# Optimization experiments

Measured on AMD Instinct MI355X. Metric: run time of the kernel, lower is better.

The kernel has to match this reference:

```python
import jax, jax.numpy as jnp
import numpy as np

N_HEADS = 8
D_MODEL = 256
HEAD_DEPTH = D_MODEL // N_HEADS
B, S = 2, 4096


def setup_inputs() -> dict:
    key = jax.random.key(0)
    ks = jax.random.split(key, 8)
    scale = 1.0 / np.sqrt(D_MODEL)
    return {
        "q": jax.random.normal(ks[0], (B, S, D_MODEL), dtype=jnp.float32),
        "k": jax.random.normal(ks[1], (B, S, D_MODEL), dtype=jnp.float32),
        "v": jax.random.normal(ks[2], (B, S, D_MODEL), dtype=jnp.float32),
        "mask": jax.random.randint(ks[3], (B, S, S), 0, 2).astype(jnp.bool_),
        "wq": jax.random.normal(ks[4], (D_MODEL, D_MODEL), dtype=jnp.float32) * scale,
        "wk": jax.random.normal(ks[5], (D_MODEL, D_MODEL), dtype=jnp.float32) * scale,
        "wv": jax.random.normal(ks[6], (D_MODEL, D_MODEL), dtype=jnp.float32) * scale,
        "w_out": jax.random.normal(ks[7], (D_MODEL, D_MODEL), dtype=jnp.float32) * scale,
    }


def _split_heads(x):
    # [B, S, D] -> [B, H, S, Dh]
    b, s, _ = x.shape
    return x.reshape(b, s, N_HEADS, HEAD_DEPTH).transpose(0, 2, 1, 3)


def reference(q, k, v, mask, wq, wk, wv, w_out):
    Q = _split_heads(q @ wq)
    K = _split_heads(k @ wk)
    V = _split_heads(v @ wv)
    # [B, H, Sq, Sk]
    scores = jnp.einsum('bhqd,bhkd->bhqk', Q, K) / jnp.sqrt(
        jnp.asarray(HEAD_DEPTH, dtype=Q.dtype))
    # mask True -> -inf, broadcast over heads
    scores = jnp.where(mask[:, None, :, :], -jnp.inf, scores)
    probs = jax.nn.softmax(scores, axis=-1)
    attn = jnp.einsum('bhqk,bhkd->bhqd', probs, V)
    attn = attn.transpose(0, 2, 1, 3).reshape(q.shape[0], -1, D_MODEL)
    return attn @ w_out
```

## Files before the change

### kernel.cpp

```cpp
#include <hip/hip_runtime.h>
#include <stdint.h>

typedef __bf16 bf16;
typedef __bf16 bf16x8 __attribute__((ext_vector_type(8)));
typedef __bf16 bf16x4 __attribute__((ext_vector_type(4)));
typedef float  f32x4  __attribute__((ext_vector_type(4)));
typedef float  float4v __attribute__((ext_vector_type(4)));

#define B_  2
#define S_  4096
#define H_  8
#define DH_ 32
#define D_  256

#define QSCALE 0.25505003984214403f

__global__ __launch_bounds__(256) void transpose_w(
    const float* __restrict__ w0, const float* __restrict__ w1,
    const float* __restrict__ w2, const float* __restrict__ w3,
    bf16* __restrict__ WT) {
  const int wsel = blockIdx.z;
  const float* W = wsel == 0 ? w0 : wsel == 1 ? w1 : wsel == 2 ? w2 : w3;
  const int k0 = blockIdx.x * 64, n0 = blockIdx.y * 64;
  __shared__ __align__(16) bf16 t[64][72];
  const int tid = threadIdx.x;
  {
    const int kk = (tid >> 4) << 2;
    const int nn = (tid & 15) << 2;
#pragma unroll
    for (int r = 0; r < 4; ++r) {
      float4v a = *(const float4v*)(W + (size_t)(k0 + kk + r) * 256 + n0 + nn);
#pragma unroll
      for (int j = 0; j < 4; ++j) t[nn + j][kk + r] = (bf16)a[j];
    }
  }
  __syncthreads();
  {
    const int ni = tid >> 2;
    const int c  = (tid & 3) * 16;
    bf16x8 o0 = *(const bf16x8*)(&t[ni][c]);
    bf16x8 o1 = *(const bf16x8*)(&t[ni][c + 8]);
    bf16* dst = WT + (size_t)wsel * 65536 + (size_t)(n0 + ni) * 256 + k0 + c;
    *(bf16x8*)dst = o0;
    *(bf16x8*)(dst + 8) = o1;
  }
}

__global__ __launch_bounds__(256) void pack_mask(const int* __restrict__ mask,
                                                 unsigned long long* __restrict__ out) {
  const int gw = blockIdx.x * 4 + (threadIdx.x >> 6);
  const int lane = threadIdx.x & 63;
  const int m = mask[(size_t)gw * 64 + lane];
  const unsigned long long bits = __ballot(m != 0);
  if (lane == 0) out[gw] = bits;
}

__global__ __launch_bounds__(256) void proj_kernel(
    const float* __restrict__ xq, const float* __restrict__ xk, const float* __restrict__ xv,
    const bf16* __restrict__ WT,
    bf16* __restrict__ Qo, bf16* __restrict__ Ko, bf16* __restrict__ Vo) {
  const int z = blockIdx.z;
  const float* X = z == 0 ? xq : (z == 1 ? xk : xv);
  const bf16* wt = WT + (size_t)z * 65536;
  const int m0 = blockIdx.x * 64, n0 = blockIdx.y * 128;
  const int tid = threadIdx.x, wave = tid >> 6, lane = tid & 63;
  const int nl = lane & 15, quad = lane >> 4;
  const int arow = m0 + wave * 16 + nl;
  const float* xrow = X + (size_t)arow * 256;

  f32x4 zero4 = {0.f, 0.f, 0.f, 0.f};
  f32x4 acc[8];
#pragma unroll
  for (int i = 0; i < 8; ++i) acc[i] = zero4;

  for (int ks = 0; ks < 8; ++ks) {
    float4v a0 = *(const float4v*)(xrow + ks * 32 + quad * 8);
    float4v a1 = *(const float4v*)(xrow + ks * 32 + quad * 8 + 4);
    bf16x8 af;
#pragma unroll
    for (int i = 0; i < 4; ++i) { af[i] = (bf16)a0[i]; af[4 + i] = (bf16)a1[i]; }
#pragma unroll
    for (int nf = 0; nf < 8; ++nf) {
      bf16x8 bfr = *(const bf16x8*)(wt + (size_t)(n0 + nf * 16 + nl) * 256 + ks * 32 + quad * 8);
      acc[nf] = __builtin_amdgcn_mfma_f32_16x16x32_bf16(af, bfr, acc[nf], 0, 0, 0);
    }
  }

  const float scale = (z == 0) ? QSCALE : 1.0f;
  bf16* Out = z == 0 ? Qo : (z == 1 ? Ko : Vo);
  const int Rbase = m0 + wave * 16 + quad * 4;
#pragma unroll
  for (int nf = 0; nf < 8; ++nf) {
    const int col = n0 + nf * 16 + nl;
    const int h = col >> 5, d = col & 31;
#pragma unroll
    for (int r = 0; r < 4; ++r) {
      const int R = Rbase + r;
      const int b = R >> 12, s = R & 4095;
      Out[(((size_t)(b * 8 + h)) * 4096 + s) * 32 + d] = (bf16)(acc[nf][r] * scale);
    }
  }
}

__global__ __launch_bounds__(256) void transpose_v(const bf16* __restrict__ Vi,
                                                   bf16* __restrict__ Vt) {
  const int bh = blockIdx.y;
  const int s0 = blockIdx.x * 64;
  __shared__ __align__(16) bf16 t[32][72];
  const int tid = threadIdx.x;
  const int si = tid >> 2, dc = (tid & 3) * 8;
  bf16x8 v = *(const bf16x8*)(Vi + ((size_t)bh * 4096 + s0 + si) * 32 + dc);
#pragma unroll
  for (int j = 0; j < 8; ++j) t[dc + j][si] = v[j];
  __syncthreads();
  const int d = tid >> 3, c = (tid & 7) * 8;
  bf16x8 o = *(const bf16x8*)(&t[d][c]);
  *(bf16x8*)(Vt + ((size_t)bh * 32 + d) * 4096 + s0 + c) = o;
}

__global__ __launch_bounds__(256) void attn_kernel(
    const bf16* __restrict__ Qg, const bf16* __restrict__ Kg,
    const bf16* __restrict__ Vtg, const unsigned long long* __restrict__ Mg,
    bf16* __restrict__ Og) {
  const int bh = blockIdx.y, b = bh >> 3, h = bh & 7;
  const int q0 = blockIdx.x * 64;
  const int tid = threadIdx.x, wave = tid >> 6, lane = tid & 63;
  const int nl = lane & 15, quad = lane >> 4;

  __shared__ __align__(16) bf16 Klds[64 * 32];
  __shared__ __align__(16) bf16 Vlds[32 * 80];
  __shared__ __align__(16) bf16 Plds[4][16 * 72];

  const int qrow = q0 + wave * 16 + nl;
  const bf16x8 qf = *(const bf16x8*)(Qg + ((size_t)bh * 4096 + qrow) * 32 + quad * 8);
  const unsigned long long* mrow = Mg + ((size_t)b * 4096 + qrow) * 64;
  const bf16* Kbase = Kg + (size_t)bh * 4096 * 32;
  const bf16* Vbase = Vtg + (size_t)bh * 32 * 4096;
  const int sd = tid >> 3, scn = (tid & 7) * 8;

  f32x4 zero4 = {0.f, 0.f, 0.f, 0.f};
  f32x4 acc0 = zero4, acc1 = zero4;
  float lsum = 0.f;

  bf16* pw = &Plds[wave][nl * 72 + 4 * quad];
  const bf16* pr = &Plds[wave][nl * 72 + quad * 8];

  for (int kt = 0; kt < 64; ++kt) {
    *(bf16x8*)(Klds + tid * 8) = *(const bf16x8*)(Kbase + (size_t)kt * 2048 + tid * 8);
    *(bf16x8*)(Vlds + sd * 80 + scn) = *(const bf16x8*)(Vbase + (size_t)sd * 4096 + kt * 64 + scn);
    __syncthreads();

    const unsigned long long mw = mrow[kt];

    f32x4 st[4];
#pragma unroll
    for (int t = 0; t < 4; ++t) {
      bf16x8 a = *(const bf16x8*)(Klds + (t * 16 + nl) * 32 + quad * 8);
      st[t] = __builtin_amdgcn_mfma_f32_16x16x32_bf16(a, qf, zero4, 0, 0, 0);
    }

#pragma unroll
    for (int t = 0; t < 4; ++t) {
      bf16x4 p4;
#pragma unroll
      for (int r = 0; r < 4; ++r) {
        const int kl = t * 16 + quad * 4 + r;
        float e = __builtin_amdgcn_exp2f(st[t][r]);
        e = ((mw >> kl) & 1ull) ? 0.f : e;
        lsum += e;
        p4[r] = (bf16)e;
      }
      *(bf16x4*)(pw + 16 * t) = p4;
    }

#pragma unroll
    for (int c = 0; c < 2; ++c) {
      bf16x8 pb  = *(const bf16x8*)(pr + c * 32);
      bf16x8 va0 = *(const bf16x8*)(Vlds + nl * 80 + c * 32 + quad * 8);
      bf16x8 va1 = *(const bf16x8*)(Vlds + (nl + 16) * 80 + c * 32 + quad * 8);
      acc0 = __builtin_amdgcn_mfma_f32_16x16x32_bf16(va0, pb, acc0, 0, 0, 0);
      acc1 = __builtin_amdgcn_mfma_f32_16x16x32_bf16(va1, pb, acc1, 0, 0, 0);
    }
    __syncthreads();
  }

  lsum += __shfl_xor(lsum, 16, 64);
  lsum += __shfl_xor(lsum, 32, 64);
  const float rl = 1.f / lsum;

  bf16x4 o0, o1;
#pragma unroll
  for (int r = 0; r < 4; ++r) { o0[r] = (bf16)(acc0[r] * rl); o1[r] = (bf16)(acc1[r] * rl); }
  bf16* obase = Og + ((size_t)(b * 4096 + qrow)) * 256 + h * 32 + quad * 4;
  *(bf16x4*)obase = o0;
  *(bf16x4*)(obase + 16) = o1;
}

__global__ __launch_bounds__(256) void gemm_out(
    const bf16* __restrict__ A, const bf16* __restrict__ WTo, float* __restrict__ C) {
  const int m0 = blockIdx.x * 64, n0 = blockIdx.y * 128;
  const int tid = threadIdx.x, wave = tid >> 6, lane = tid & 63;
  const int nl = lane & 15, quad = lane >> 4;
  const int arow = m0 + wave * 16 + nl;

  f32x4 zero4 = {0.f, 0.f, 0.f, 0.f};
  f32x4 acc[8];
#pragma unroll
  for (int i = 0; i < 8; ++i) acc[i] = zero4;

  for (int ks = 0; ks < 8; ++ks) {
    bf16x8 af = *(const bf16x8*)(A + (size_t)arow * 256 + ks * 32 + quad * 8);
#pragma unroll
    for (int nf = 0; nf < 8; ++nf) {
      bf16x8 bfr = *(const bf16x8*)(WTo + (size_t)(n0 + nf * 16 + nl) * 256 + ks * 32 + quad * 8);
      acc[nf] = __builtin_amdgcn_mfma_f32_16x16x32_bf16(af, bfr, acc[nf], 0, 0, 0);
    }
  }
  const int Rbase = m0 + wave * 16 + quad * 4;
#pragma unroll
  for (int nf = 0; nf < 8; ++nf)
#pragma unroll
    for (int r = 0; r < 4; ++r)
      C[(size_t)(Rbase + r) * 256 + n0 + nf * 16 + nl] = acc[nf][r];
}

extern "C" void kernel_launch(void* const* d_in, const int* in_sizes, int n_in,
                              void* d_out, int out_size, void* d_ws, size_t ws_size,
                              hipStream_t stream) {
  const float* q  = (const float*)d_in[0];
  const float* k  = (const float*)d_in[1];
  const float* v  = (const float*)d_in[2];
  const int*  mask = (const int*)d_in[3];
  const float* wq = (const float*)d_in[4];
  const float* wk = (const float*)d_in[5];
  const float* wv = (const float*)d_in[6];
  const float* wo = (const float*)d_in[7];
  float* out = (float*)d_out;

  uint8_t* ws = (uint8_t*)d_ws;
  bf16* WT = (bf16*)ws;
  bf16* Qb = (bf16*)(ws + (512u << 10));
  bf16* Kb = Qb + 2097152;
  bf16* Vb = Kb + 2097152;
  bf16* Vt = Vb + 2097152;
  unsigned long long* Mb = (unsigned long long*)((uint8_t*)(Vt + 2097152));
  bf16* Ao = (bf16*)((uint8_t*)Mb + (4u << 20));

  transpose_w<<<dim3(4, 4, 4), 256, 0, stream>>>(wq, wk, wv, wo, WT);
  pack_mask<<<dim3(131072), 256, 0, stream>>>(mask, Mb);
  proj_kernel<<<dim3(128, 2, 3), 256, 0, stream>>>(q, k, v, WT, Qb, Kb, Vb);
  transpose_v<<<dim3(64, 16), 256, 0, stream>>>(Vb, Vt);
  attn_kernel<<<dim3(64, 16), 256, 0, stream>>>(Qb, Kb, Vt, Mb, Ao);
  gemm_out<<<dim3(128, 2), 256, 0, stream>>>(Ao, WT + 3 * 65536, out);
}
```

Measured before the change: 378.3 us.

## Fuse V transpose into projection, widen attention K tile, batch mask packing

The V projection now writes directly in transposed layout, so the separate transpose_v kernel and its buffer are gone. The attention kernel processes 128 keys per iteration, which halves the number of barriers. It masks with a bitfield AND instead of a select and computes the softmax denominator with an extra MFMA against a ones vector instead of a scalar sum and shuffles. pack_mask has each wave ballot 16 words and store them with wide writes, cutting the block count from 131072 to 8192. The changes add LDS use and an extra MFMA per chunk, and the row sum is now accumulated from bf16-rounded probabilities.

```diff
diff --git a/kernel.cpp b/kernel.cpp
--- a/kernel.cpp
+++ b/kernel.cpp
@@ -6,12 +6,8 @@
 typedef __bf16 bf16x4 __attribute__((ext_vector_type(4)));
 typedef float  f32x4  __attribute__((ext_vector_type(4)));
 typedef float  float4v __attribute__((ext_vector_type(4)));
-
-#define B_  2
-#define S_  4096
-#define H_  8
-#define DH_ 32
-#define D_  256
+typedef unsigned int uint;
+typedef unsigned long long ull;
 
 #define QSCALE 0.25505003984214403f
 
@@ -47,18 +43,24 @@
 }
 
 __global__ __launch_bounds__(256) void pack_mask(const int* __restrict__ mask,
-                                                 unsigned long long* __restrict__ out) {
-  const int gw = blockIdx.x * 4 + (threadIdx.x >> 6);
+                                                 ull* __restrict__ out) {
+  const int wid = blockIdx.x * 4 + (threadIdx.x >> 6);
   const int lane = threadIdx.x & 63;
-  const int m = mask[(size_t)gw * 64 + lane];
-  const unsigned long long bits = __ballot(m != 0);
-  if (lane == 0) out[gw] = bits;
+  const size_t base = (size_t)wid * 1024 + lane;
+  ull b[16];
+#pragma unroll
+  for (int j = 0; j < 16; ++j) b[j] = __ballot(mask[base + 64 * j] != 0);
+  if (lane == 0) {
+    ulonglong2* o = (ulonglong2*)(out + (size_t)wid * 16);
+#pragma unroll
+    for (int j = 0; j < 8; ++j) { ulonglong2 v; v.x = b[2 * j]; v.y = b[2 * j + 1]; o[j] = v; }
+  }
 }
 
 __global__ __launch_bounds__(256) void proj_kernel(
     const float* __restrict__ xq, const float* __restrict__ xk, const float* __restrict__ xv,
     const bf16* __restrict__ WT,
-    bf16* __restrict__ Qo, bf16* __restrict__ Ko, bf16* __restrict__ Vo) {
+    bf16* __restrict__ Qo, bf16* __restrict__ Ko, bf16* __restrict__ Vt) {
   const int z = blockIdx.z;
   const float* X = z == 0 ? xq : (z == 1 ? xk : xv);
   const bf16* wt = WT + (size_t)z * 65536;
@@ -86,112 +88,121 @@
     }
   }
 
-  const float scale = (z == 0) ? QSCALE : 1.0f;
-  bf16* Out = z == 0 ? Qo : (z == 1 ? Ko : Vo);
   const int Rbase = m0 + wave * 16 + quad * 4;
-#pragma unroll
-  for (int nf = 0; nf < 8; ++nf) {
-    const int col = n0 + nf * 16 + nl;
-    const int h = col >> 5, d = col & 31;
-#pragma unroll
-    for (int r = 0; r < 4; ++r) {
-      const int R = Rbase + r;
-      const int b = R >> 12, s = R & 4095;
-      Out[(((size_t)(b * 8 + h)) * 4096 + s) * 32 + d] = (bf16)(acc[nf][r] * scale);
-    }
-  }
-}
-
-__global__ __launch_bounds__(256) void transpose_v(const bf16* __restrict__ Vi,
-                                                   bf16* __restrict__ Vt) {
-  const int bh = blockIdx.y;
-  const int s0 = blockIdx.x * 64;
-  __shared__ __align__(16) bf16 t[32][72];
-  const int tid = threadIdx.x;
-  const int si = tid >> 2, dc = (tid & 3) * 8;
-  bf16x8 v = *(const bf16x8*)(Vi + ((size_t)bh * 4096 + s0 + si) * 32 + dc);
-#pragma unroll
-  for (int j = 0; j < 8; ++j) t[dc + j][si] = v[j];
-  __syncthreads();
-  const int d = tid >> 3, c = (tid & 7) * 8;
-  bf16x8 o = *(const bf16x8*)(&t[d][c]);
-  *(bf16x8*)(Vt + ((size_t)bh * 32 + d) * 4096 + s0 + c) = o;
-}
-
-__global__ __launch_bounds__(256) void attn_kernel(
+  if (z == 2) {
+    const int b = Rbase >> 12, s = Rbase & 4095;
+#pragma unroll
+    for (int nf = 0; nf < 8; ++nf) {
+      const int col = n0 + nf * 16 + nl;
+      const int h = col >> 5, d = col & 31;
+      bf16x4 o;
+#pragma unroll
+      for (int r = 0; r < 4; ++r) o[r] = (bf16)acc[nf][r];
+      *(bf16x4*)(Vt + (((size_t)(b * 8 + h)) * 32 + d) * 4096 + s) = o;
+    }
+  } else {
+    const float scale = (z == 0) ? QSCALE : 1.0f;
+    bf16* Out = z == 0 ? Qo : Ko;
+#pragma unroll
+    for (int nf = 0; nf < 8; ++nf) {
+      const int col = n0 + nf * 16 + nl;
+      const int h = col >> 5, d = col & 31;
+#pragma unroll
+      for (int r = 0; r < 4; ++r) {
+        const int R = Rbase + r;
+        const int b = R >> 12, s = R & 4095;
+        Out[(((size_t)(b * 8 + h)) * 4096 + s) * 32 + d] = (bf16)(acc[nf][r] * scale);
+      }
+    }
+  }
+}
+
+__global__ __launch_bounds__(256, 6) void attn_kernel(
     const bf16* __restrict__ Qg, const bf16* __restrict__ Kg,
-    const bf16* __restrict__ Vtg, const unsigned long long* __restrict__ Mg,
+    const bf16* __restrict__ Vtg, const uint* __restrict__ Mg,
     bf16* __restrict__ Og) {
   const int bh = blockIdx.y, b = bh >> 3, h = bh & 7;
   const int q0 = blockIdx.x * 64;
   const int tid = threadIdx.x, wave = tid >> 6, lane = tid & 63;
-  const int nl = lane & 15, quad = lane >> 4;
-
-  __shared__ __align__(16) bf16 Klds[64 * 32];
-  __shared__ __align__(16) bf16 Vlds[32 * 80];
+  const int nl = lane & 15, quad = lane >> 4, q4 = quad * 4;
+
+  __shared__ __align__(16) bf16 Klds[128 * 32];
+  __shared__ __align__(16) bf16 Vlds[32 * 136];
   __shared__ __align__(16) bf16 Plds[4][16 * 72];
 
   const int qrow = q0 + wave * 16 + nl;
   const bf16x8 qf = *(const bf16x8*)(Qg + ((size_t)bh * 4096 + qrow) * 32 + quad * 8);
-  const unsigned long long* mrow = Mg + ((size_t)b * 4096 + qrow) * 64;
+  const uint* mrow = Mg + ((size_t)b * 4096 + qrow) * 128;
   const bf16* Kbase = Kg + (size_t)bh * 4096 * 32;
   const bf16* Vbase = Vtg + (size_t)bh * 32 * 4096;
-  const int sd = tid >> 3, scn = (tid & 7) * 8;
 
   f32x4 zero4 = {0.f, 0.f, 0.f, 0.f};
-  f32x4 acc0 = zero4, acc1 = zero4;
-  float lsum = 0.f;
-
-  bf16* pw = &Plds[wave][nl * 72 + 4 * quad];
+  f32x4 acc0 = zero4, acc1 = zero4, accl = zero4;
+  bf16x8 ones;
+#pragma unroll
+  for (int i = 0; i < 8; ++i) ones[i] = (bf16)1.0f;
+
+  bf16* pw = &Plds[wave][nl * 72 + q4];
   const bf16* pr = &Plds[wave][nl * 72 + quad * 8];
-
-  for (int kt = 0; kt < 64; ++kt) {
-    *(bf16x8*)(Klds + tid * 8) = *(const bf16x8*)(Kbase + (size_t)kt * 2048 + tid * 8);
-    *(bf16x8*)(Vlds + sd * 80 + scn) = *(const bf16x8*)(Vbase + (size_t)sd * 4096 + kt * 64 + scn);
+  const int vd = tid >> 4, vk = (tid & 15) * 8;
+
+  for (int kt = 0; kt < 32; ++kt) {
+    const bf16* kc = Kbase + kt * 4096;
+    *(bf16x8*)(Klds + tid * 8)        = *(const bf16x8*)(kc + tid * 8);
+    *(bf16x8*)(Klds + 2048 + tid * 8) = *(const bf16x8*)(kc + 2048 + tid * 8);
+    const bf16* vc = Vbase + kt * 128 + vk;
+    *(bf16x8*)(Vlds + vd * 136 + vk)        = *(const bf16x8*)(vc + (size_t)vd * 4096);
+    *(bf16x8*)(Vlds + (vd + 16) * 136 + vk) = *(const bf16x8*)(vc + (size_t)(vd + 16) * 4096);
     __syncthreads();
 
-    const unsigned long long mw = mrow[kt];
-
-    f32x4 st[4];
-#pragma unroll
-    for (int t = 0; t < 4; ++t) {
-      bf16x8 a = *(const bf16x8*)(Klds + (t * 16 + nl) * 32 + quad * 8);
-      st[t] = __builtin_amdgcn_mfma_f32_16x16x32_bf16(a, qf, zero4, 0, 0, 0);
-    }
-
-#pragma unroll
-    for (int t = 0; t < 4; ++t) {
-      bf16x4 p4;
-#pragma unroll
-      for (int r = 0; r < 4; ++r) {
-        const int kl = t * 16 + quad * 4 + r;
-        float e = __builtin_amdgcn_exp2f(st[t][r]);
-        e = ((mw >> kl) & 1ull) ? 0.f : e;
-        lsum += e;
-        p4[r] = (bf16)e;
-      }
-      *(bf16x4*)(pw + 16 * t) = p4;
-    }
-
-#pragma unroll
-    for (int c = 0; c < 2; ++c) {
-      bf16x8 pb  = *(const bf16x8*)(pr + c * 32);
-      bf16x8 va0 = *(const bf16x8*)(Vlds + nl * 80 + c * 32 + quad * 8);
-      bf16x8 va1 = *(const bf16x8*)(Vlds + (nl + 16) * 80 + c * 32 + quad * 8);
-      acc0 = __builtin_amdgcn_mfma_f32_16x16x32_bf16(va0, pb, acc0, 0, 0, 0);
-      acc1 = __builtin_amdgcn_mfma_f32_16x16x32_bf16(va1, pb, acc1, 0, 0, 0);
+    const uint4 mq = *(const uint4*)(mrow + kt * 4);
+
+#pragma unroll
+    for (int h2 = 0; h2 < 2; ++h2) {
+      const uint ks0 = (~(h2 ? mq.z : mq.x)) >> q4;
+      const uint ks1 = (~(h2 ? mq.w : mq.y)) >> q4;
+
+      f32x4 st[4];
+#pragma unroll
+      for (int t = 0; t < 4; ++t) {
+        bf16x8 a = *(const bf16x8*)(Klds + ((h2 * 4 + t) * 16 + nl) * 32 + quad * 8);
+        st[t] = __builtin_amdgcn_mfma_f32_16x16x32_bf16(a, qf, zero4, 0, 0, 0);
+      }
+
+#pragma unroll
+      for (int t = 0; t < 4; ++t) {
+        const uint ks = (t < 2) ? ks0 : ks1;
+        const int off = (t & 1) * 16;
+        bf16x4 p4;
+#pragma unroll
+        for (int r = 0; r < 4; ++r) {
+          float e = __builtin_amdgcn_exp2f(st[t][r]);
+          uint keep = (uint)__builtin_amdgcn_sbfe((int)ks, off + r, 1);
+          e = __uint_as_float(__float_as_uint(e) & keep);
+          p4[r] = (bf16)e;
+        }
+        *(bf16x4*)(pw + 16 * t) = p4;
+      }
+
+#pragma unroll
+      for (int c = 0; c < 2; ++c) {
+        bf16x8 pb  = *(const bf16x8*)(pr + c * 32);
+        bf16x8 va0 = *(const bf16x8*)(Vlds + nl * 136 + h2 * 64 + c * 32 + quad * 8);
+        bf16x8 va1 = *(const bf16x8*)(Vlds + (nl + 16) * 136 + h2 * 64 + c * 32 + quad * 8);
+        acc0 = __builtin_amdgcn_mfma_f32_16x16x32_bf16(va0, pb, acc0, 0, 0, 0);
+        acc1 = __builtin_amdgcn_mfma_f32_16x16x32_bf16(va1, pb, acc1, 0, 0, 0);
+        accl = __builtin_amdgcn_mfma_f32_16x16x32_bf16(ones, pb, accl, 0, 0, 0);
+      }
     }
     __syncthreads();
   }
 
-  lsum += __shfl_xor(lsum, 16, 64);
-  lsum += __shfl_xor(lsum, 32, 64);
-  const float rl = 1.f / lsum;
+  const float rl = 1.0f / accl[0];
 
   bf16x4 o0, o1;
 #pragma unroll
   for (int r = 0; r < 4; ++r) { o0[r] = (bf16)(acc0[r] * rl); o1[r] = (bf16)(acc1[r] * rl); }
-  bf16* obase = Og + ((size_t)(b * 4096 + qrow)) * 256 + h * 32 + quad * 4;
+  bf16* obase = Og + ((size_t)(b * 4096 + qrow)) * 256 + h * 32 + q4;
   *(bf16x4*)obase = o0;
   *(bf16x4*)(obase + 16) = o1;
 }
@@ -241,15 +252,13 @@
   bf16* WT = (bf16*)ws;
   bf16* Qb = (bf16*)(ws + (512u << 10));
   bf16* Kb = Qb + 2097152;
-  bf16* Vb = Kb + 2097152;
-  bf16* Vt = Vb + 2097152;
-  unsigned long long* Mb = (unsigned long long*)((uint8_t*)(Vt + 2097152));
+  bf16* Vt = Kb + 2097152;
+  ull*  Mb = (ull*)((uint8_t*)(Vt + 2097152));
   bf16* Ao = (bf16*)((uint8_t*)Mb + (4u << 20));
 
   transpose_w<<<dim3(4, 4, 4), 256, 0, stream>>>(wq, wk, wv, wo, WT);
-  pack_mask<<<dim3(131072), 256, 0, stream>>>(mask, Mb);
-  proj_kernel<<<dim3(128, 2, 3), 256, 0, stream>>>(q, k, v, WT, Qb, Kb, Vb);
-  transpose_v<<<dim3(64, 16), 256, 0, stream>>>(Vb, Vt);
-  attn_kernel<<<dim3(64, 16), 256, 0, stream>>>(Qb, Kb, Vt, Mb, Ao);
+  pack_mask<<<dim3(8192), 256, 0, stream>>>(mask, Mb);
+  proj_kernel<<<dim3(128, 2, 3), 256, 0, stream>>>(q, k, v, WT, Qb, Kb, Vt);
+  attn_kernel<<<dim3(64, 16), 256, 0, stream>>>(Qb, Kb, Vt, (const uint*)Mb, Ao);
   gemm_out<<<dim3(128, 2), 256, 0, stream>>>(Ao, WT + 3 * 65536, out);
 }
```

Measured after the change: 349.3 us. 1.08x faster.
